# Performance work log

Hardware: AMD Instinct MI355X
Metric: run time of the kernel (lower is better)

## Reference

```python
import jax, jax.numpy as jnp
import numpy as np

T, H, I, E, Z, TOPK = 1024, 1024, 512, 32, 8, 4
ROUTED_SCALING = 1.0


def setup_inputs() -> dict:
    key = jax.random.key(0)
    k1, k2, k3, k4 = jax.random.split(key, 4)
    return {
        "hidden_states": jax.random.normal(k1, (T, H), jnp.float32),
        "router_w": jax.random.normal(k2, (E + Z, H), jnp.float32) * 0.02,
        "correction_bias": jnp.zeros((E + Z,), jnp.float32),
        "w_gate_up": jax.random.normal(k3, (E, 2 * I, H), jnp.float32) * 0.02,
        "w_down": jax.random.normal(k4, (E, H, I), jnp.float32) * 0.02,
        "top_k": TOPK,
    }


def reference(hidden_states, router_w, correction_bias, w_gate_up, w_down, top_k):
    # hidden_states: [T, H]; router_w: [E+Z, H]; w_gate_up: [E, 2I, H]; w_down: [E, H, I]
    t, h = hidden_states.shape
    e = w_gate_up.shape[0]
    i = w_down.shape[2]
    # --- router (float32, no bias; correction bias only affects selection) ---
    logits = jnp.einsum("th,eh->te", hidden_states.astype(jnp.float32), router_w)
    scores = jax.nn.softmax(logits, axis=-1)                     # [T, E+Z]
    _, idx = jax.lax.top_k(scores + correction_bias[None, :], top_k)  # [T, k]
    w = jnp.take_along_axis(scores, idx, axis=1) * ROUTED_SCALING     # renormalize=False
    # combine matrix [T, E+Z] (sparse top-k scattered dense)
    comb = jnp.zeros((t, scores.shape[1]), jnp.float32)
    comb = comb.at[jnp.arange(t)[:, None], idx].add(w)
    comb_routed = comb[:, :e].astype(hidden_states.dtype)        # [T, E]
    zero_w = comb[:, e:].sum(-1).astype(hidden_states.dtype)     # [T] identity zero-experts
    # --- grouped SiLU-gated expert MLPs (dense all-experts reference) ---
    gu = jnp.einsum("th,eih->eti", hidden_states, w_gate_up)     # [E, T, 2I]
    hmid = jax.nn.silu(gu[..., :i]) * gu[..., i:]                # [E, T, I]
    ye = jnp.einsum("eti,ehi->eth", hmid, w_down)                # [E, T, H]
    out = jnp.einsum("te,eth->th", comb_routed, ye)
    out = out + zero_w[:, None] * hidden_states
    return out
```

## Files before the change

kernel.cpp:

```cpp
#include <hip/hip_runtime.h>
#include <hip/hip_cooperative_groups.h>
#include <hip/hip_bf16.h>
#include <math.h>

namespace cg = cooperative_groups;

#define TT   1024
#define HH   1024
#define II   512
#define EE   32
#define NE   40
#define TOPK 4
#define CAP  1024

#define GM  128
#define GNP 32
#define GK  32
#define KP  40
#define DN  64

typedef __attribute__((ext_vector_type(4))) short short4v;
typedef __attribute__((ext_vector_type(8))) short short8v;
typedef __attribute__((ext_vector_type(4))) float floatx4;

static __device__ __forceinline__ short f2bf(float f) {
    unsigned u = __float_as_uint(f);
    unsigned r = (u + 0x7fffu + ((u >> 16) & 1u)) >> 16;
    return (short)(r & 0xffffu);
}
static __device__ __forceinline__ float bf2f(short s) {
    return __uint_as_float(((unsigned)(unsigned short)s) << 16);
}
#if defined(__has_builtin)
#if __has_builtin(__builtin_amdgcn_cvt_pk_bf16_f32)
#define HAVE_PK_BF16 1
#endif
#endif
static __device__ __forceinline__ unsigned pk2(float a, float b) {
#ifdef HAVE_PK_BF16
    typedef __attribute__((ext_vector_type(2))) __bf16 bf2t;
    union { bf2t v; unsigned u; } cv;
    cv.v = __builtin_amdgcn_cvt_pk_bf16_f32(a, b);
    return cv.u;
#else
    return (unsigned)(unsigned short)f2bf(a) | ((unsigned)(unsigned short)f2bf(b) << 16);
#endif
}
static __device__ __forceinline__ short4v cvt4(float4 v) {
    union { unsigned u[2]; short4v s; } cv;
    cv.u[0] = pk2(v.x, v.y); cv.u[1] = pk2(v.z, v.w);
    return cv.s;
}

struct SMem {
    short As[GM * KP];
    short Bs[2 * GNP * KP];
    int   sl[GM];
    float wvs[GM];
};


static __device__ __forceinline__ void phaseA(
    const int bx, const int tid,
    const float* __restrict__ x, const float* __restrict__ rw,
    const float* __restrict__ bias,
    float* __restrict__ topk_w, float* __restrict__ zero_w,
    int* __restrict__ kexp, int* __restrict__ counts,
    int* __restrict__ slots, short* __restrict__ xb)
{
    const int lane = tid & 63;
    const int w    = tid >> 6;

    if (w < 2) {
        const int t = bx * 2 + w;
        float xv[16];
        #pragma unroll
        for (int i = 0; i < 16; ++i) xv[i] = x[(size_t)t * HH + 64 * i + lane];

        float mylogit = -INFINITY;
        for (int e0 = 0; e0 < NE; e0 += 4) {
            const float* r0 = rw + (size_t)e0 * HH;
            float p[4] = { 0.f, 0.f, 0.f, 0.f };
            #pragma unroll
            for (int i = 0; i < 16; ++i) {
                int h = 64 * i + lane;
                #pragma unroll
                for (int j = 0; j < 4; ++j) p[j] += xv[i] * r0[(size_t)j * HH + h];
            }
            #pragma unroll
            for (int j = 0; j < 4; ++j) {
                #pragma unroll
                for (int off = 32; off > 0; off >>= 1) p[j] += __shfl_xor(p[j], off);
                if (lane == e0 + j) mylogit = p[j];
            }
        }

        float m = mylogit;
        #pragma unroll
        for (int off = 32; off > 0; off >>= 1) m = fmaxf(m, __shfl_xor(m, off));
        float pexp = (lane < NE) ? expf(mylogit - m) : 0.f;
        float s = pexp;
        #pragma unroll
        for (int off = 32; off > 0; off >>= 1) s += __shfl_xor(s, off);
        const float score = pexp / s;

        float val = (lane < NE) ? score + bias[lane] : -INFINITY;
        int   kidx[TOPK];
        float kw[TOPK];
        #pragma unroll
        for (int k = 0; k < TOPK; ++k) {
            float v = val; int idx = lane;
            #pragma unroll
            for (int off = 32; off > 0; off >>= 1) {
                float ov = __shfl_xor(v, off);
                int   oi = __shfl_xor(idx, off);
                if (ov > v || (ov == v && oi < idx)) { v = ov; idx = oi; }
            }
            kidx[k] = idx;
            kw[k]   = __shfl(score, idx);
            if (lane == idx) val = -INFINITY;
        }

        if (lane == 0) {
            float zw = 0.f;
            #pragma unroll
            for (int k = 0; k < TOPK; ++k) {
                int slot = t * TOPK + k;
                topk_w[slot] = kw[k];
                kexp[slot]   = kidx[k];
                if (kidx[k] < EE) {
                    int pos = atomicAdd(&counts[kidx[k]], 1);
                    slots[kidx[k] * CAP + pos] = slot;
                } else {
                    zw += kw[k];
                }
            }
            zero_w[t] = zw;
        }
    } else {
        const int t = bx * 2 + (w - 2);
        const float4* xr = (const float4*)(x + (size_t)t * HH);
        short4v* xbr = (short4v*)(xb + (size_t)t * HH);
        #pragma unroll
        for (int i = 0; i < 4; ++i) xbr[lane + 64 * i] = cvt4(xr[lane + 64 * i]);
    }
}

static __device__ __forceinline__ void phaseB(
    const int bx, const int tid, SMem* sm,
    const short* __restrict__ xb, const float* __restrict__ wgu,
    const int* __restrict__ counts, const int* __restrict__ slots,
    const float* __restrict__ topk_w, short* __restrict__ hmid)
{
    const int e      = bx >> 4;
    const int c_base = (bx & 15) * GNP;
    const int cnt    = counts[e];
    const float* wb  = wgu + (size_t)e * (2 * II) * HH;

    const int lane = tid & 63;
    const int w    = tid >> 6;
    const int wy   = w & 1;
    const int wx   = w >> 1;
    const int quad = lane >> 4;
    const int mcol = lane & 15;

    for (int m_base = 0; m_base < cnt; m_base += GM) {
        if (tid < GM) {
            int m = m_base + tid;
            int s = (m < cnt) ? slots[e * CAP + m] : -1;
            sm->sl[tid]  = s;
            sm->wvs[tid] = (s >= 0) ? topk_w[s] : 0.f;
        }
        __syncthreads();

        const int kcA = tid & 3;
        int rowA[2]; int slA[2]; const short* pA[2];
        #pragma unroll
        for (int it = 0; it < 2; ++it) {
            rowA[it] = (tid >> 2) + 64 * it;
            int s = sm->sl[rowA[it]];
            slA[it] = s;
            pA[it] = xb + (size_t)((s >= 0 ? s : 0) >> 2) * HH + kcA * 8;
        }
        const int kq = tid & 7;
        int rowB[2]; const float* pB[2];
        #pragma unroll
        for (int it = 0; it < 2; ++it) {
            rowB[it] = (tid >> 3) + 32 * it;
            int grow = (rowB[it] < GNP) ? (c_base + rowB[it])
                                        : (II + c_base + rowB[it] - GNP);
            pB[it] = wb + (size_t)grow * HH + kq * 4;
        }

        floatx4 accg[4] = {};
        floatx4 accu[4] = {};
        short8v pa[2]; float4 pb[2];
        const short8v szv = { 0,0,0,0,0,0,0,0 };

        #pragma unroll
        for (int it = 0; it < 2; ++it) pa[it] = (slA[it] >= 0) ? *(const short8v*)(pA[it]) : szv;
        #pragma unroll
        for (int it = 0; it < 2; ++it) pb[it] = *(const float4*)(pB[it]);

        for (int k0 = 0; k0 < HH; k0 += GK) {
            #pragma unroll
            for (int it = 0; it < 2; ++it) *(short8v*)&sm->As[rowA[it] * KP + kcA * 8] = pa[it];
            #pragma unroll
            for (int it = 0; it < 2; ++it) *(short4v*)&sm->Bs[rowB[it] * KP + kq * 4] = cvt4(pb[it]);
            __syncthreads();

            const int kn = k0 + GK;
            if (kn < HH) {
                #pragma unroll
                for (int it = 0; it < 2; ++it) pa[it] = (slA[it] >= 0) ? *(const short8v*)(pA[it] + kn) : szv;
                #pragma unroll
                for (int it = 0; it < 2; ++it) pb[it] = *(const float4*)(pB[it] + kn);
            }

            short8v a[4], bg, bu;
            #pragma unroll
            for (int i = 0; i < 4; ++i)
                a[i] = *(const short8v*)&sm->As[(wy * 64 + i * 16 + mcol) * KP + quad * 8];
            bg = *(const short8v*)&sm->Bs[(wx * 16 + mcol) * KP + quad * 8];
            bu = *(const short8v*)&sm->Bs[(GNP + wx * 16 + mcol) * KP + quad * 8];
            #pragma unroll
            for (int i = 0; i < 4; ++i) {
                accg[i] = __builtin_amdgcn_mfma_f32_16x16x32_bf16(a[i], bg, accg[i], 0, 0, 0);
                accu[i] = __builtin_amdgcn_mfma_f32_16x16x32_bf16(a[i], bu, accu[i], 0, 0, 0);
            }
            __syncthreads();
        }

        #pragma unroll
        for (int i = 0; i < 4; ++i) {
            #pragma unroll
            for (int r = 0; r < 4; ++r) {
                int m = wy * 64 + i * 16 + quad * 4 + r;
                int s = sm->sl[m];
                if (s < 0) continue;
                float g = accg[i][r], u = accu[i][r];
                float valf = sm->wvs[m] * g * u / (1.f + __expf(-g));
                hmid[(size_t)s * II + c_base + wx * 16 + mcol] = f2bf(valf);
            }
        }
        __syncthreads();
    }
}

static __device__ __forceinline__ void phaseC(
    const int bx, const int tid, SMem* sm,
    const short* __restrict__ hmid, const float* __restrict__ wd,
    const int* __restrict__ counts, const int* __restrict__ slots,
    short* __restrict__ ydown)
{
    const int e      = bx >> 4;
    const int n_base = (bx & 15) * DN;
    const int cnt    = counts[e];
    const float* wb  = wd + (size_t)e * HH * II;

    const int lane = tid & 63;
    const int w    = tid >> 6;
    const int wy   = w & 1;
    const int wx   = w >> 1;
    const int quad = lane >> 4;
    const int mcol = lane & 15;

    for (int m_base = 0; m_base < cnt; m_base += GM) {
        if (tid < GM) {
            int m = m_base + tid;
            sm->sl[tid] = (m < cnt) ? slots[e * CAP + m] : -1;
        }
        __syncthreads();

        const int kcA = tid & 3;
        int rowA[2]; int slA[2]; const short* pA[2];
        #pragma unroll
        for (int it = 0; it < 2; ++it) {
            rowA[it] = (tid >> 2) + 64 * it;
            int s = sm->sl[rowA[it]];
            slA[it] = s;
            pA[it] = hmid + (size_t)(s >= 0 ? s : 0) * II + kcA * 8;
        }
        const int kq = tid & 7;
        int rowB[2]; const float* pB[2];
        #pragma unroll
        for (int it = 0; it < 2; ++it) {
            rowB[it] = (tid >> 3) + 32 * it;
            pB[it] = wb + (size_t)(n_base + rowB[it]) * II + kq * 4;
        }

        floatx4 acc[4][2] = {};
        short8v pa[2]; float4 pb[2];
        const short8v szv = { 0,0,0,0,0,0,0,0 };

        #pragma unroll
        for (int it = 0; it < 2; ++it) pa[it] = (slA[it] >= 0) ? *(const short8v*)(pA[it]) : szv;
        #pragma unroll
        for (int it = 0; it < 2; ++it) pb[it] = *(const float4*)(pB[it]);

        for (int k0 = 0; k0 < II; k0 += GK) {
            #pragma unroll
            for (int it = 0; it < 2; ++it) *(short8v*)&sm->As[rowA[it] * KP + kcA * 8] = pa[it];
            #pragma unroll
            for (int it = 0; it < 2; ++it) *(short4v*)&sm->Bs[rowB[it] * KP + kq * 4] = cvt4(pb[it]);
            __syncthreads();

            const int kn = k0 + GK;
            if (kn < II) {
                #pragma unroll
                for (int it = 0; it < 2; ++it) pa[it] = (slA[it] >= 0) ? *(const short8v*)(pA[it] + kn) : szv;
                #pragma unroll
                for (int it = 0; it < 2; ++it) pb[it] = *(const float4*)(pB[it] + kn);
            }

            short8v a[4], b[2];
            #pragma unroll
            for (int i = 0; i < 4; ++i)
                a[i] = *(const short8v*)&sm->As[(wy * 64 + i * 16 + mcol) * KP + quad * 8];
            #pragma unroll
            for (int j = 0; j < 2; ++j)
                b[j] = *(const short8v*)&sm->Bs[(wx * 32 + j * 16 + mcol) * KP + quad * 8];
            #pragma unroll
            for (int i = 0; i < 4; ++i)
                #pragma unroll
                for (int j = 0; j < 2; ++j)
                    acc[i][j] = __builtin_amdgcn_mfma_f32_16x16x32_bf16(a[i], b[j], acc[i][j], 0, 0, 0);
            __syncthreads();
        }

        #pragma unroll
        for (int i = 0; i < 4; ++i) {
            #pragma unroll
            for (int r = 0; r < 4; ++r) {
                int m = wy * 64 + i * 16 + quad * 4 + r;
                int s = sm->sl[m];
                if (s < 0) continue;
                short* yrow = ydown + (size_t)s * HH + n_base + wx * 32;
                #pragma unroll
                for (int j = 0; j < 2; ++j)
                    yrow[j * 16 + mcol] = f2bf(acc[i][j][r]);
            }
        }
        __syncthreads();
    }
}

static __device__ __forceinline__ void phaseD(
    const int bx, const int tid,
    const float* __restrict__ x, const short* __restrict__ ydown,
    const int* __restrict__ kexp, const float* __restrict__ zero_w,
    float* __restrict__ out)
{
    #pragma unroll
    for (int j = 0; j < 2; ++j) {
        const int t = bx * 2 + j;
        const float4 xvv = ((const float4*)(x + (size_t)t * HH))[tid];
        const float zw = zero_w[t];
        float4 o;
        o.x = zw * xvv.x; o.y = zw * xvv.y; o.z = zw * xvv.z; o.w = zw * xvv.w;
        #pragma unroll
        for (int k = 0; k < TOPK; ++k) {
            int slot = t * TOPK + k;
            if (kexp[slot] < EE) {
                short4v y = *(const short4v*)&ydown[(size_t)slot * HH + tid * 4];
                o.x += bf2f(y[0]); o.y += bf2f(y[1]);
                o.z += bf2f(y[2]); o.w += bf2f(y[3]);
            }
        }
        ((float4*)(out + (size_t)t * HH))[tid] = o;
    }
}

__global__ __launch_bounds__(256, 2) void fused_moe(
    const float* __restrict__ x, const float* __restrict__ rw,
    const float* __restrict__ bias, const float* __restrict__ wgu,
    const float* __restrict__ wd, float* __restrict__ out,
    int* __restrict__ counts, float* __restrict__ topk_w,
    float* __restrict__ zero_w, int* __restrict__ kexp,
    int* __restrict__ slots, short* __restrict__ xb,
    short* __restrict__ hmid, short* __restrict__ ydown)
{
    cg::grid_group grid = cg::this_grid();
    __shared__ SMem sm;
    const int bx = blockIdx.x, tid = threadIdx.x;

    phaseA(bx, tid, x, rw, bias, topk_w, zero_w, kexp, counts, slots, xb);
    __threadfence(); grid.sync();
    phaseB(bx, tid, &sm, xb, wgu, counts, slots, topk_w, hmid);
    __threadfence(); grid.sync();
    phaseC(bx, tid, &sm, hmid, wd, counts, slots, ydown);
    __threadfence(); grid.sync();
    phaseD(bx, tid, x, ydown, kexp, zero_w, out);
}

__global__ __launch_bounds__(256, 2) void kA(
    const float* __restrict__ x, const float* __restrict__ rw,
    const float* __restrict__ bias, float* __restrict__ topk_w,
    float* __restrict__ zero_w, int* __restrict__ kexp,
    int* __restrict__ counts, int* __restrict__ slots, short* __restrict__ xb)
{
    phaseA(blockIdx.x, threadIdx.x, x, rw, bias, topk_w, zero_w, kexp, counts, slots, xb);
}
__global__ __launch_bounds__(256, 2) void kB(
    const short* __restrict__ xb, const float* __restrict__ wgu,
    const int* __restrict__ counts, const int* __restrict__ slots,
    const float* __restrict__ topk_w, short* __restrict__ hmid)
{
    __shared__ SMem sm;
    phaseB(blockIdx.x, threadIdx.x, &sm, xb, wgu, counts, slots, topk_w, hmid);
}
__global__ __launch_bounds__(256, 2) void kC(
    const short* __restrict__ hmid, const float* __restrict__ wd,
    const int* __restrict__ counts, const int* __restrict__ slots,
    short* __restrict__ ydown)
{
    __shared__ SMem sm;
    phaseC(blockIdx.x, threadIdx.x, &sm, hmid, wd, counts, slots, ydown);
}
__global__ __launch_bounds__(256, 2) void kD(
    const float* __restrict__ x, const short* __restrict__ ydown,
    const int* __restrict__ kexp, const float* __restrict__ zero_w,
    float* __restrict__ out)
{
    phaseD(blockIdx.x, threadIdx.x, x, ydown, kexp, zero_w, out);
}

extern "C" void kernel_launch(void* const* d_in, const int* in_sizes, int n_in,
                              void* d_out, int out_size, void* d_ws, size_t ws_size,
                              hipStream_t stream) {
    const float* x    = (const float*)d_in[0];
    const float* rw   = (const float*)d_in[1];
    const float* bias = (const float*)d_in[2];
    const float* wgu  = (const float*)d_in[3];
    const float* wd   = (const float*)d_in[4];
    float* out = (float*)d_out;

    char* ws = (char*)d_ws;
    int*   counts = (int*)ws;
    float* topk_w = (float*)(ws + 1024);
    float* zero_w = (float*)(ws + 17408);
    int*   kexp   = (int*)(ws + 21504);
    int*   slots  = (int*)(ws + 40960);
    short* xb     = (short*)(ws + 262144);
    short* hmid   = (short*)(ws + 2359296);
    short* ydown  = (short*)(ws + 6553600);

    hipMemsetAsync(counts, 0, EE * sizeof(int), stream);

    int nb = 0;
    hipError_t qerr = hipOccupancyMaxActiveBlocksPerMultiprocessor(&nb, fused_moe, 256, 0);
    bool launched = false;
    if (qerr == hipSuccess && nb >= 2) {
        void* args[] = {
            (void*)&x, (void*)&rw, (void*)&bias, (void*)&wgu, (void*)&wd,
            (void*)&out, (void*)&counts, (void*)&topk_w, (void*)&zero_w,
            (void*)&kexp, (void*)&slots, (void*)&xb, (void*)&hmid, (void*)&ydown
        };
        hipError_t lerr = hipLaunchCooperativeKernel((const void*)fused_moe,
                                                     dim3(512), dim3(256),
                                                     args, 0, stream);
        launched = (lerr == hipSuccess);
    }
    if (!launched) {
        kA<<<dim3(512), dim3(256), 0, stream>>>(x, rw, bias, topk_w, zero_w, kexp, counts, slots, xb);
        kB<<<dim3(512), dim3(256), 0, stream>>>(xb, wgu, counts, slots, topk_w, hmid);
        kC<<<dim3(512), dim3(256), 0, stream>>>(hmid, wd, counts, slots, ydown);
        kD<<<dim3(512), dim3(256), 0, stream>>>(x, ydown, kexp, zero_w, out);
    }
}
```

Before: 311.3 us.

## Load MFMA operands directly from global memory, dropping LDS staging and barriers

Both expert GEMM phases stop staging A and B tiles through shared memory with double-buffered register prefetch and two barriers per K step. Each lane now loads its MFMA fragments straight from global memory (bf16 activations, fp32 weights converted in-register) and the K loop is unrolled by two. This removes LDS traffic and synchronisation, but each wave redundantly fetches data that other waves share. Rows are 4 KB or 2 KB apart, so the loads are less coalesced and rely on the L2 cache.

```diff
diff --git a/kernel.cpp b/kernel.cpp
--- a/kernel.cpp
+++ b/kernel.cpp
@@ -16,7 +16,6 @@
 #define GM  128
 #define GNP 32
 #define GK  32
-#define KP  40
 #define DN  64
 
 typedef __attribute__((ext_vector_type(4))) short short4v;
@@ -51,10 +50,14 @@
     cv.u[0] = pk2(v.x, v.y); cv.u[1] = pk2(v.z, v.w);
     return cv.s;
 }
+static __device__ __forceinline__ short8v pack8(float4 a, float4 b) {
+    union { unsigned u[4]; short8v s; } cv;
+    cv.u[0] = pk2(a.x, a.y); cv.u[1] = pk2(a.z, a.w);
+    cv.u[2] = pk2(b.x, b.y); cv.u[3] = pk2(b.z, b.w);
+    return cv.s;
+}
 
 struct SMem {
-    short As[GM * KP];
-    short Bs[2 * GNP * KP];
     int   sl[GM];
     float wvs[GM];
 };
@@ -164,6 +167,9 @@
     const int quad = lane >> 4;
     const int mcol = lane & 15;
 
+    const float* pg = wb + (size_t)(c_base + wx * 16 + mcol) * HH + quad * 8;
+    const float* pu = pg + (size_t)II * HH;
+
     for (int m_base = 0; m_base < cnt; m_base += GM) {
         if (tid < GM) {
             int m = m_base + tid;
@@ -173,62 +179,32 @@
         }
         __syncthreads();
 
-        const int kcA = tid & 3;
-        int rowA[2]; int slA[2]; const short* pA[2];
-        #pragma unroll
-        for (int it = 0; it < 2; ++it) {
-            rowA[it] = (tid >> 2) + 64 * it;
-            int s = sm->sl[rowA[it]];
-            slA[it] = s;
-            pA[it] = xb + (size_t)((s >= 0 ? s : 0) >> 2) * HH + kcA * 8;
-        }
-        const int kq = tid & 7;
-        int rowB[2]; const float* pB[2];
-        #pragma unroll
-        for (int it = 0; it < 2; ++it) {
-            rowB[it] = (tid >> 3) + 32 * it;
-            int grow = (rowB[it] < GNP) ? (c_base + rowB[it])
-                                        : (II + c_base + rowB[it] - GNP);
-            pB[it] = wb + (size_t)grow * HH + kq * 4;
+        const short* pa[4];
+        #pragma unroll
+        for (int i = 0; i < 4; ++i) {
+            int s = sm->sl[wy * 64 + i * 16 + mcol];
+            pa[i] = xb + (size_t)(s >= 0 ? (s >> 2) : 0) * HH + quad * 8;
         }
 
         floatx4 accg[4] = {};
         floatx4 accu[4] = {};
-        short8v pa[2]; float4 pb[2];
-        const short8v szv = { 0,0,0,0,0,0,0,0 };
-
-        #pragma unroll
-        for (int it = 0; it < 2; ++it) pa[it] = (slA[it] >= 0) ? *(const short8v*)(pA[it]) : szv;
-        #pragma unroll
-        for (int it = 0; it < 2; ++it) pb[it] = *(const float4*)(pB[it]);
-
+
+        #pragma unroll 2
         for (int k0 = 0; k0 < HH; k0 += GK) {
-            #pragma unroll
-            for (int it = 0; it < 2; ++it) *(short8v*)&sm->As[rowA[it] * KP + kcA * 8] = pa[it];
-            #pragma unroll
-            for (int it = 0; it < 2; ++it) *(short4v*)&sm->Bs[rowB[it] * KP + kq * 4] = cvt4(pb[it]);
-            __syncthreads();
-
-            const int kn = k0 + GK;
-            if (kn < HH) {
-                #pragma unroll
-                for (int it = 0; it < 2; ++it) pa[it] = (slA[it] >= 0) ? *(const short8v*)(pA[it] + kn) : szv;
-                #pragma unroll
-                for (int it = 0; it < 2; ++it) pb[it] = *(const float4*)(pB[it] + kn);
-            }
-
-            short8v a[4], bg, bu;
-            #pragma unroll
-            for (int i = 0; i < 4; ++i)
-                a[i] = *(const short8v*)&sm->As[(wy * 64 + i * 16 + mcol) * KP + quad * 8];
-            bg = *(const short8v*)&sm->Bs[(wx * 16 + mcol) * KP + quad * 8];
-            bu = *(const short8v*)&sm->Bs[(GNP + wx * 16 + mcol) * KP + quad * 8];
+            short8v a[4];
+            #pragma unroll
+            for (int i = 0; i < 4; ++i) a[i] = *(const short8v*)(pa[i] + k0);
+            float4 g0 = *(const float4*)(pg + k0);
+            float4 g1 = *(const float4*)(pg + k0 + 4);
+            float4 u0 = *(const float4*)(pu + k0);
+            float4 u1 = *(const float4*)(pu + k0 + 4);
+            short8v bg = pack8(g0, g1);
+            short8v bu = pack8(u0, u1);
             #pragma unroll
             for (int i = 0; i < 4; ++i) {
                 accg[i] = __builtin_amdgcn_mfma_f32_16x16x32_bf16(a[i], bg, accg[i], 0, 0, 0);
                 accu[i] = __builtin_amdgcn_mfma_f32_16x16x32_bf16(a[i], bu, accu[i], 0, 0, 0);
             }
-            __syncthreads();
         }
 
         #pragma unroll
@@ -265,6 +241,9 @@
     const int quad = lane >> 4;
     const int mcol = lane & 15;
 
+    const float* pb0 = wb + (size_t)(n_base + wx * 32 + mcol) * II + quad * 8;
+    const float* pb1 = pb0 + (size_t)16 * II;
+
     for (int m_base = 0; m_base < cnt; m_base += GM) {
         if (tid < GM) {
             int m = m_base + tid;
@@ -272,60 +251,31 @@
         }
         __syncthreads();
 
-        const int kcA = tid & 3;
-        int rowA[2]; int slA[2]; const short* pA[2];
-        #pragma unroll
-        for (int it = 0; it < 2; ++it) {
-            rowA[it] = (tid >> 2) + 64 * it;
-            int s = sm->sl[rowA[it]];
-            slA[it] = s;
-            pA[it] = hmid + (size_t)(s >= 0 ? s : 0) * II + kcA * 8;
-        }
-        const int kq = tid & 7;
-        int rowB[2]; const float* pB[2];
-        #pragma unroll
-        for (int it = 0; it < 2; ++it) {
-            rowB[it] = (tid >> 3) + 32 * it;
-            pB[it] = wb + (size_t)(n_base + rowB[it]) * II + kq * 4;
+        const short* pa[4];
+        #pragma unroll
+        for (int i = 0; i < 4; ++i) {
+            int s = sm->sl[wy * 64 + i * 16 + mcol];
+            pa[i] = hmid + (size_t)(s >= 0 ? s : 0) * II + quad * 8;
         }
 
         floatx4 acc[4][2] = {};
-        short8v pa[2]; float4 pb[2];
-        const short8v szv = { 0,0,0,0,0,0,0,0 };
-
-        #pragma unroll
-        for (int it = 0; it < 2; ++it) pa[it] = (slA[it] >= 0) ? *(const short8v*)(pA[it]) : szv;
-        #pragma unroll
-        for (int it = 0; it < 2; ++it) pb[it] = *(const float4*)(pB[it]);
-
+
+        #pragma unroll 2
         for (int k0 = 0; k0 < II; k0 += GK) {
-            #pragma unroll
-            for (int it = 0; it < 2; ++it) *(short8v*)&sm->As[rowA[it] * KP + kcA * 8] = pa[it];
-            #pragma unroll
-            for (int it = 0; it < 2; ++it) *(short4v*)&sm->Bs[rowB[it] * KP + kq * 4] = cvt4(pb[it]);
-            __syncthreads();
-
-            const int kn = k0 + GK;
-            if (kn < II) {
-                #pragma unroll
-                for (int it = 0; it < 2; ++it) pa[it] = (slA[it] >= 0) ? *(const short8v*)(pA[it] + kn) : szv;
-                #pragma unroll
-                for (int it = 0; it < 2; ++it) pb[it] = *(const float4*)(pB[it] + kn);
-            }
-
-            short8v a[4], b[2];
-            #pragma unroll
-            for (int i = 0; i < 4; ++i)
-                a[i] = *(const short8v*)&sm->As[(wy * 64 + i * 16 + mcol) * KP + quad * 8];
-            #pragma unroll
-            for (int j = 0; j < 2; ++j)
-                b[j] = *(const short8v*)&sm->Bs[(wx * 32 + j * 16 + mcol) * KP + quad * 8];
-            #pragma unroll
-            for (int i = 0; i < 4; ++i)
-                #pragma unroll
-                for (int j = 0; j < 2; ++j)
-                    acc[i][j] = __builtin_amdgcn_mfma_f32_16x16x32_bf16(a[i], b[j], acc[i][j], 0, 0, 0);
-            __syncthreads();
+            short8v a[4];
+            #pragma unroll
+            for (int i = 0; i < 4; ++i) a[i] = *(const short8v*)(pa[i] + k0);
+            float4 b00 = *(const float4*)(pb0 + k0);
+            float4 b01 = *(const float4*)(pb0 + k0 + 4);
+            float4 b10 = *(const float4*)(pb1 + k0);
+            float4 b11 = *(const float4*)(pb1 + k0 + 4);
+            short8v b0 = pack8(b00, b01);
+            short8v b1 = pack8(b10, b11);
+            #pragma unroll
+            for (int i = 0; i < 4; ++i) {
+                acc[i][0] = __builtin_amdgcn_mfma_f32_16x16x32_bf16(a[i], b0, acc[i][0], 0, 0, 0);
+                acc[i][1] = __builtin_amdgcn_mfma_f32_16x16x32_bf16(a[i], b1, acc[i][1], 0, 0, 0);
+            }
         }
 
         #pragma unroll
```

Result: slower. 340.6 us (+9.4%).
